# Optimization experiments

Hardware: AMD Instinct MI355X
Metric: run time of the kernel (lower is better)

Reference implementation:

```python
import jax, jax.numpy as jnp
import numpy as np

DIM = 512
HEADS = 8
DIM_HEAD = 64
INNER = HEADS * DIM_HEAD
SCALE = DIM_HEAD ** -0.5


def setup_inputs() -> dict:
    key = jax.random.key(0)
    ks = jax.random.split(key, 7)
    B, N = 8, 1024
    x = jax.random.normal(ks[0], (B, N, DIM), dtype=jnp.float32)
    rel_pos_bias = jax.random.normal(ks[1], (HEADS, N, N), dtype=jnp.float32) * 0.02
    w_qkv = jax.random.normal(ks[2], (DIM, 3 * INNER), dtype=jnp.float32) * (DIM ** -0.5)
    w_out = jax.random.normal(ks[3], (INNER, DIM), dtype=jnp.float32) * (INNER ** -0.5)
    b_out = jnp.zeros((DIM,), dtype=jnp.float32)
    ln_gamma = jnp.ones((DIM,), dtype=jnp.float32)
    ln_beta = jnp.zeros((DIM,), dtype=jnp.float32)
    return {"x": x, "rel_pos_bias": rel_pos_bias, "w_qkv": w_qkv,
            "w_out": w_out, "b_out": b_out, "ln_gamma": ln_gamma, "ln_beta": ln_beta}


def _layernorm(x, gamma, beta, eps=1e-5):
    mu = jnp.mean(x, axis=-1, keepdims=True)
    var = jnp.var(x, axis=-1, keepdims=True)
    return (x - mu) * jax.lax.rsqrt(var + eps) * gamma + beta


def reference(x, rel_pos_bias, w_qkv, w_out, b_out, ln_gamma, ln_beta):
    B, N, _ = x.shape
    xn = _layernorm(x, ln_gamma, ln_beta)
    qkv = xn @ w_qkv  # [B,N,3*INNER]
    q, k, v = jnp.split(qkv, 3, axis=-1)
    # b n (h d) -> b h n d
    reshape = lambda t: t.reshape(B, N, HEADS, DIM_HEAD).transpose(0, 2, 1, 3)
    q, k, v = reshape(q) * SCALE, reshape(k), reshape(v)
    sim = jnp.einsum('bhid,bhjd->bhij', q, k)
    sim = sim + rel_pos_bias  # broadcast [h,N,N] over batch
    attn = jax.nn.softmax(sim, axis=-1)
    out = jnp.einsum('bhij,bhjd->bhid', attn, v)
    out = out.transpose(0, 2, 1, 3).reshape(B, N, INNER)
    return out @ w_out + b_out
```

## Files before the change

### kernel.cpp

```cpp
#include <hip/hip_runtime.h>
#include <hip/hip_bf16.h>

#define DIM 512
#define HEADS 8
#define DHEAD 64
#define INNER 512
#define NSEQ 1024
#define BATCH 8
#define MROWS (BATCH*NSEQ)
#define QK_SCALE 0.125f
#define LOG2E 1.44269504f

typedef __attribute__((ext_vector_type(4))) float f32x4;
typedef __attribute__((ext_vector_type(8))) short short8;
typedef unsigned short ushort_t;

__device__ inline ushort_t f2bf(float f) {
    __hip_bfloat16 h = __float2bfloat16(f);
    return *reinterpret_cast<ushort_t*>(&h);
}
__device__ inline float bf2f(ushort_t u) {
    union { unsigned int i; float f; } c; c.i = ((unsigned int)u) << 16; return c.f;
}
__device__ inline float fast_exp2(float x) {
    float r; asm("v_exp_f32 %0, %1" : "=v"(r) : "v"(x)); return r;
}

#define GLD16(gsrc, ldst) __builtin_amdgcn_global_load_lds( \
    (const __attribute__((address_space(1))) void*)(gsrc), \
    (__attribute__((address_space(3))) void*)(ldst), 16, 0, 0)

__device__ inline void tc_tile(const float* __restrict__ w, ushort_t* __restrict__ wt,
        int ncols, int n0, int k0, int t, ushort_t (*T)[72]) {
    int kr = t >> 2;
    int nc = (t & 3) * 16;
    const float4* src = (const float4*)(w + (size_t)(k0 + kr) * ncols + n0 + nc);
    float4 f0 = src[0], f1 = src[1], f2 = src[2], f3 = src[3];
    ushort_t tmp[16];
    tmp[0]=f2bf(f0.x); tmp[1]=f2bf(f0.y); tmp[2]=f2bf(f0.z); tmp[3]=f2bf(f0.w);
    tmp[4]=f2bf(f1.x); tmp[5]=f2bf(f1.y); tmp[6]=f2bf(f1.z); tmp[7]=f2bf(f1.w);
    tmp[8]=f2bf(f2.x); tmp[9]=f2bf(f2.y); tmp[10]=f2bf(f2.z); tmp[11]=f2bf(f2.w);
    tmp[12]=f2bf(f3.x); tmp[13]=f2bf(f3.y); tmp[14]=f2bf(f3.z); tmp[15]=f2bf(f3.w);
    *(uint4*)&T[kr][nc]     = *(uint4*)&tmp[0];
    *(uint4*)&T[kr][nc + 8] = *(uint4*)&tmp[8];
    __syncthreads();
    int nr = t >> 2;
    int kc = (t & 3) * 16;
    ushort_t o[16];
    for (int j = 0; j < 16; j++) o[j] = T[kc + j][nr];
    ushort_t* dst = wt + (size_t)(n0 + nr) * 512 + k0 + kc;
    *(uint4*)(dst)     = *(uint4*)&o[0];
    *(uint4*)(dst + 8) = *(uint4*)&o[8];
}

__global__ __launch_bounds__(256) void prep_kernel(
        const float* __restrict__ x, const float* __restrict__ gamma,
        const float* __restrict__ beta, ushort_t* __restrict__ xn,
        const float* __restrict__ w_qkv, ushort_t* __restrict__ wqkvT,
        const float* __restrict__ w_out, ushort_t* __restrict__ woutT,
        const float* __restrict__ bias, ushort_t* __restrict__ biasb) {
    __shared__ ushort_t T[64][72];
    int bid = blockIdx.x;
    int t = threadIdx.x;
    if (bid < 2048) {
        int row = bid * 4 + (t >> 6);
        int lane = t & 63;
        const float4* xr = (const float4*)(x + (size_t)row * DIM);
        float4 a0 = xr[lane];
        float4 a1 = xr[lane + 64];
        float s  = a0.x + a0.y + a0.z + a0.w + a1.x + a1.y + a1.z + a1.w;
        float ss = a0.x*a0.x + a0.y*a0.y + a0.z*a0.z + a0.w*a0.w
                 + a1.x*a1.x + a1.y*a1.y + a1.z*a1.z + a1.w*a1.w;
        for (int off = 1; off < 64; off <<= 1) {
            s  += __shfl_xor(s, off);
            ss += __shfl_xor(ss, off);
        }
        float mean = s * (1.0f / DIM);
        float var  = ss * (1.0f / DIM) - mean * mean;
        float inv  = rsqrtf(var + 1e-5f);
        const float4* g4 = (const float4*)gamma;
        const float4* b4 = (const float4*)beta;
        float4 g0 = g4[lane], g1 = g4[lane + 64];
        float4 be0 = b4[lane], be1 = b4[lane + 64];
        ushort4 o0, o1;
        o0.x = f2bf((a0.x - mean) * inv * g0.x + be0.x);
        o0.y = f2bf((a0.y - mean) * inv * g0.y + be0.y);
        o0.z = f2bf((a0.z - mean) * inv * g0.z + be0.z);
        o0.w = f2bf((a0.w - mean) * inv * g0.w + be0.w);
        o1.x = f2bf((a1.x - mean) * inv * g1.x + be1.x);
        o1.y = f2bf((a1.y - mean) * inv * g1.y + be1.y);
        o1.z = f2bf((a1.z - mean) * inv * g1.z + be1.z);
        o1.w = f2bf((a1.w - mean) * inv * g1.w + be1.w);
        ushort4* outr = (ushort4*)(xn + (size_t)row * DIM);
        outr[lane] = o0;
        outr[lane + 64] = o1;
    } else if (bid < 2240) {
        int rel = bid - 2048;
        tc_tile(w_qkv, wqkvT, 1536, (rel % 24) * 64, (rel / 24) * 64, t, T);
    } else if (bid < 2304) {
        int rel = bid - 2240;
        tc_tile(w_out, woutT, 512, (rel % 8) * 64, (rel / 8) * 64, t, T);
    } else {
        int rel = bid - 2304;
        int i = rel * 256 + t;
        float4 v = ((const float4*)bias)[i];
        ushort4 o;
        o.x = f2bf(v.x * LOG2E); o.y = f2bf(v.y * LOG2E);
        o.z = f2bf(v.z * LOG2E); o.w = f2bf(v.w * LOG2E);
        ((ushort4*)biasb)[i] = o;
    }
}

__global__ __launch_bounds__(256) void gemm_qkv(
        const ushort_t* __restrict__ A, const ushort_t* __restrict__ Bt,
        ushort_t* __restrict__ qb, ushort_t* __restrict__ kb, ushort_t* __restrict__ vt) {
    __shared__ ushort_t Als[128][32];
    __shared__ ushort_t Bls[128][32];
    __shared__ ushort_t Tw[4][64][72];
    int t = threadIdx.x, lane = t & 63, w = t >> 6;
    int bm = blockIdx.y, bn = blockIdx.x;
    int wm = w >> 1, wn = w & 1;
    int l15 = lane & 15, l4 = lane >> 4;
    int lr = lane >> 2, lc = (lane & 3) * 8;

    const ushort_t* gA = A  + (size_t)(bm * 128) * DIM;
    const ushort_t* gB = Bt + (size_t)(bn * 128) * DIM;

    f32x4 acc[4][4] = {};

    GLD16(gA + (size_t)(w*32      + lr) * DIM + lc, &Als[w*32][0]);
    GLD16(gA + (size_t)(w*32 + 16 + lr) * DIM + lc, &Als[w*32 + 16][0]);
    GLD16(gB + (size_t)(w*32      + lr) * DIM + lc, &Bls[w*32][0]);
    GLD16(gB + (size_t)(w*32 + 16 + lr) * DIM + lc, &Bls[w*32 + 16][0]);

    for (int kt = 0; kt < DIM / 32; ++kt) {
        __syncthreads();
        short8 af[4], bfr[4];
        for (int mi = 0; mi < 4; mi++) af[mi]  = *(const short8*)&Als[wm*64 + mi*16 + l15][l4*8];
        for (int ni = 0; ni < 4; ni++) bfr[ni] = *(const short8*)&Bls[wn*64 + ni*16 + l15][l4*8];
        __syncthreads();
        if (kt + 1 < DIM / 32) {
            int ko = (kt + 1) * 32;
            GLD16(gA + (size_t)(w*32      + lr) * DIM + ko + lc, &Als[w*32][0]);
            GLD16(gA + (size_t)(w*32 + 16 + lr) * DIM + ko + lc, &Als[w*32 + 16][0]);
            GLD16(gB + (size_t)(w*32      + lr) * DIM + ko + lc, &Bls[w*32][0]);
            GLD16(gB + (size_t)(w*32 + 16 + lr) * DIM + ko + lc, &Bls[w*32 + 16][0]);
        }
        for (int mi = 0; mi < 4; mi++)
            for (int ni = 0; ni < 4; ni++)
                acc[mi][ni] = __builtin_amdgcn_mfma_f32_16x16x32_bf16(bfr[ni], af[mi], acc[mi][ni], 0, 0, 0);
    }

    int c0 = bn*128 + wn*64;
    int part = c0 >> 9;
    int h = (c0 & 511) >> 6;
    int R0 = bm*128 + wm*64;
    int b = R0 >> 10;
    int i0 = R0 & 1023;
    size_t bh = (size_t)(b * HEADS + h);

    if (part == 2) {
        for (int mi = 0; mi < 4; mi++)
            for (int ni = 0; ni < 4; ni++) {
                f32x4 v = acc[mi][ni];
                for (int j = 0; j < 4; j++)
                    Tw[w][ni*16 + l4*4 + j][mi*16 + l15] = f2bf(v[j]);
            }
    } else {
        float qs = (part == 0) ? (QK_SCALE * LOG2E) : 1.0f;
        for (int mi = 0; mi < 4; mi++)
            for (int ni = 0; ni < 4; ni++) {
                f32x4 v = acc[mi][ni];
                ushort4 o;
                o.x = f2bf(v[0] * qs); o.y = f2bf(v[1] * qs);
                o.z = f2bf(v[2] * qs); o.w = f2bf(v[3] * qs);
                *(ushort4*)&Tw[w][mi*16 + l15][ni*16 + l4*4] = o;
            }
    }
    __syncthreads();

    int rr = lane >> 3;
    int cc = (lane & 7) * 8;
    if (part == 2) {
        for (int s = 0; s < 8; s++) {
            int dloc = s*8 + rr;
            uint4 val = *(const uint4*)&Tw[w][dloc][cc];
            *(uint4*)(vt + (bh * DHEAD + dloc) * NSEQ + i0 + cc) = val;
        }
    } else {
        ushort_t* dst = (part == 0) ? qb : kb;
        for (int s = 0; s < 8; s++) {
            int iloc = s*8 + rr;
            uint4 val = *(const uint4*)&Tw[w][iloc][cc];
            *(uint4*)(dst + (bh * NSEQ + (i0 + iloc)) * DHEAD + cc) = val;
        }
    }
}

__global__ __launch_bounds__(256) void gemm_out(
        const ushort_t* __restrict__ A, const ushort_t* __restrict__ Bt,
        float* __restrict__ outp, const float* __restrict__ bvec) {
    __shared__ ushort_t Als[128][32];
    __shared__ ushort_t Bls[64][32];
    __shared__ float Twf[4][64][36];
    int t = threadIdx.x, lane = t & 63, w = t >> 6;
    int bm = blockIdx.y, bn = blockIdx.x;
    int wm = w >> 1, wn = w & 1;
    int l15 = lane & 15, l4 = lane >> 4;
    int lr = lane >> 2, lc = (lane & 3) * 8;

    const ushort_t* gA = A  + (size_t)(bm * 128) * DIM;
    const ushort_t* gB = Bt + (size_t)(bn * 64) * DIM;

    f32x4 acc[4][2] = {};

    GLD16(gA + (size_t)(w*32      + lr) * DIM + lc, &Als[w*32][0]);
    GLD16(gA + (size_t)(w*32 + 16 + lr) * DIM + lc, &Als[w*32 + 16][0]);
    GLD16(gB + (size_t)(w*16 + lr) * DIM + lc, &Bls[w*16][0]);

    for (int kt = 0; kt < DIM / 32; ++kt) {
        __syncthreads();
        short8 af[4], bfr[2];
        for (int mi = 0; mi < 4; mi++) af[mi]  = *(const short8*)&Als[wm*64 + mi*16 + l15][l4*8];
        for (int ni = 0; ni < 2; ni++) bfr[ni] = *(const short8*)&Bls[wn*32 + ni*16 + l15][l4*8];
        __syncthreads();
        if (kt + 1 < DIM / 32) {
            int ko = (kt + 1) * 32;
            GLD16(gA + (size_t)(w*32      + lr) * DIM + ko + lc, &Als[w*32][0]);
            GLD16(gA + (size_t)(w*32 + 16 + lr) * DIM + ko + lc, &Als[w*32 + 16][0]);
            GLD16(gB + (size_t)(w*16 + lr) * DIM + ko + lc, &Bls[w*16][0]);
        }
        for (int mi = 0; mi < 4; mi++)
            for (int ni = 0; ni < 2; ni++)
                acc[mi][ni] = __builtin_amdgcn_mfma_f32_16x16x32_bf16(bfr[ni], af[mi], acc[mi][ni], 0, 0, 0);
    }

    int C0 = bn*64 + wn*32;
    int R0 = bm*128 + wm*64;
    for (int mi = 0; mi < 4; mi++)
        for (int ni = 0; ni < 2; ni++) {
            int c = C0 + ni*16 + l4*4;
            float4 bv = *(const float4*)(bvec + c);
            f32x4 v = acc[mi][ni];
            float4 o2;
            o2.x = v[0] + bv.x; o2.y = v[1] + bv.y;
            o2.z = v[2] + bv.z; o2.w = v[3] + bv.w;
            *(float4*)&Twf[w][mi*16 + l15][ni*16 + l4*4] = o2;
        }
    __syncthreads();

    int rr = lane >> 3;
    int cc = (lane & 7) * 4;
    for (int s = 0; s < 8; s++) {
        int iloc = s*8 + rr;
        float4 val = *(const float4*)&Twf[w][iloc][cc];
        *(float4*)(outp + (size_t)(R0 + iloc) * DIM + C0 + cc) = val;
    }
}

__global__ __launch_bounds__(256) void attn_kernel(
        const ushort_t* __restrict__ q, const ushort_t* __restrict__ k,
        const ushort_t* __restrict__ vt, const ushort_t* __restrict__ biasb,
        ushort_t* __restrict__ attno) {
    __shared__ ushort_t Kls[64][72];
    __shared__ ushort_t Vtls[64][72];
    __shared__ ushort_t Pls[4][16][72];
    int t = threadIdx.x, lane = t & 63, w = t >> 6;
    int l15 = lane & 15, l4 = lane >> 4;
    int bid = blockIdx.x;
    int xcd = bid & 7, s2 = bid >> 3;
    int g = xcd * 16 + (s2 >> 3);
    int b = s2 & 7;
    int h = g & 7;
    int q0 = (g >> 3) * 64;
    size_t bh = (size_t)(b * HEADS + h);
    const ushort_t* qp = q  + (bh * NSEQ + q0 + w*16) * DHEAD;
    const ushort_t* kp = k  + bh * NSEQ * DHEAD;
    const ushort_t* vp = vt + bh * DHEAD * NSEQ;
    int qrow = q0 + w*16 + l15;
    const ushort_t* bp = biasb + ((size_t)h * NSEQ + qrow) * NSEQ;

    short8 bq[2];
    bq[0] = *(const short8*)(qp + l15*DHEAD + l4*8);
    bq[1] = *(const short8*)(qp + l15*DHEAD + l4*8 + 32);

    f32x4 o[4] = {};
    float mrun = -INFINITY, lrun = 0.f;

    int srow = t >> 2, sc = (t & 3) * 16;

    uint4 kreg0, kreg1, vreg0, vreg1;
    ushort4 cb[4], nb[4];
    {
        const ushort_t* ks0 = kp + (size_t)srow * DHEAD + sc;
        const ushort_t* vs0 = vp + (size_t)srow * NSEQ + sc;
        kreg0 = *(const uint4*)(ks0);
        kreg1 = *(const uint4*)(ks0 + 8);
        vreg0 = *(const uint4*)(vs0);
        vreg1 = *(const uint4*)(vs0 + 8);
        for (int ni = 0; ni < 4; ni++)
            cb[ni] = *(const ushort4*)(bp + ni*16 + l4*4);
    }

    for (int kt = 0; kt < NSEQ / 64; ++kt) {
        __syncthreads();
        *(uint4*)&Kls[srow][sc]      = kreg0;
        *(uint4*)&Kls[srow][sc + 8]  = kreg1;
        *(uint4*)&Vtls[srow][sc]     = vreg0;
        *(uint4*)&Vtls[srow][sc + 8] = vreg1;
        __syncthreads();

        if (kt + 1 < NSEQ / 64) {
            const ushort_t* ksn = kp + (size_t)((kt+1)*64 + srow) * DHEAD + sc;
            const ushort_t* vsn = vp + (size_t)srow * NSEQ + (kt+1)*64 + sc;
            kreg0 = *(const uint4*)(ksn);
            kreg1 = *(const uint4*)(ksn + 8);
            vreg0 = *(const uint4*)(vsn);
            vreg1 = *(const uint4*)(vsn + 8);
        }

        f32x4 s[4];
        __builtin_amdgcn_s_setprio(1);
        for (int ni = 0; ni < 4; ni++) {
            f32x4 z = {};
            short8 ak0 = *(const short8*)&Kls[ni*16 + l15][l4*8];
            short8 ak1 = *(const short8*)&Kls[ni*16 + l15][l4*8 + 32];
            z = __builtin_amdgcn_mfma_f32_16x16x32_bf16(ak0, bq[0], z, 0, 0, 0);
            z = __builtin_amdgcn_mfma_f32_16x16x32_bf16(ak1, bq[1], z, 0, 0, 0);
            s[ni] = z;
        }
        __builtin_amdgcn_s_setprio(0);

        float p[16];
        float mj = -INFINITY;
        for (int ni = 0; ni < 4; ni++) {
            ushort4 b4 = cb[ni];
            float v0 = s[ni][0] + bf2f(b4.x);
            float v1 = s[ni][1] + bf2f(b4.y);
            float v2 = s[ni][2] + bf2f(b4.z);
            float v3 = s[ni][3] + bf2f(b4.w);
            p[ni*4+0] = v0; p[ni*4+1] = v1; p[ni*4+2] = v2; p[ni*4+3] = v3;
            mj = fmaxf(mj, fmaxf(fmaxf(v0, v1), fmaxf(v2, v3)));
        }
        mj = fmaxf(mj, __shfl_xor(mj, 16));
        mj = fmaxf(mj, __shfl_xor(mj, 32));
        if (kt + 1 < NSEQ / 64) {
            for (int ni = 0; ni < 4; ni++)
                nb[ni] = *(const ushort4*)(bp + (kt+1)*64 + ni*16 + l4*4);
        }
        if (!__all(mj <= mrun + 8.f)) {
            float mnew = fmaxf(mrun, mj);
            float scl = fast_exp2(mrun - mnew);
            lrun *= scl;
            for (int di = 0; di < 4; di++) o[di] *= scl;
            mrun = mnew;
        }
        float rs = 0.f;
        for (int i = 0; i < 16; i++) {
            p[i] = fast_exp2(p[i] - mrun);
            rs += p[i];
        }
        rs += __shfl_xor(rs, 16);
        rs += __shfl_xor(rs, 32);
        lrun += rs;

        for (int ni = 0; ni < 4; ni++) {
            ushort4 pk;
            pk.x = f2bf(p[ni*4+0]); pk.y = f2bf(p[ni*4+1]);
            pk.z = f2bf(p[ni*4+2]); pk.w = f2bf(p[ni*4+3]);
            *(ushort4*)&Pls[w][l15][ni*16 + l4*4] = pk;
        }

        __builtin_amdgcn_s_setprio(1);
        for (int ks2 = 0; ks2 < 2; ks2++) {
            short8 pb = *(const short8*)&Pls[w][l15][ks2*32 + l4*8];
            for (int di = 0; di < 4; di++) {
                short8 av = *(const short8*)&Vtls[di*16 + l15][ks2*32 + l4*8];
                o[di] = __builtin_amdgcn_mfma_f32_16x16x32_bf16(av, pb, o[di], 0, 0, 0);
            }
        }
        __builtin_amdgcn_s_setprio(0);

        for (int ni = 0; ni < 4; ni++) cb[ni] = nb[ni];
    }

    float inv = 1.0f / lrun;
    for (int di = 0; di < 4; di++) {
        ushort4 ov;
        ov.x = f2bf(o[di][0] * inv);
        ov.y = f2bf(o[di][1] * inv);
        ov.z = f2bf(o[di][2] * inv);
        ov.w = f2bf(o[di][3] * inv);
        *(ushort4*)(attno + ((size_t)(b*NSEQ + qrow)) * INNER + h*DHEAD + di*16 + l4*4) = ov;
    }
}

extern "C" void kernel_launch(void* const* d_in, const int* in_sizes, int n_in,
                              void* d_out, int out_size, void* d_ws, size_t ws_size,
                              hipStream_t stream) {
    (void)in_sizes; (void)n_in; (void)out_size; (void)ws_size;
    const float* x      = (const float*)d_in[0];
    const float* bias   = (const float*)d_in[1];
    const float* w_qkv  = (const float*)d_in[2];
    const float* w_out  = (const float*)d_in[3];
    const float* b_out  = (const float*)d_in[4];
    const float* gamma  = (const float*)d_in[5];
    const float* beta   = (const float*)d_in[6];
    float* out = (float*)d_out;

    ushort_t* xn    = (ushort_t*)d_ws;
    ushort_t* wqkvT = xn + (size_t)MROWS * DIM;
    ushort_t* woutT = wqkvT + (size_t)1536 * 512;
    ushort_t* qb    = woutT + (size_t)512 * 512;
    ushort_t* kb    = qb + (size_t)MROWS * INNER;
    ushort_t* vt    = kb + (size_t)MROWS * INNER;
    ushort_t* attn  = vt + (size_t)MROWS * INNER;
    ushort_t* biasb = attn + (size_t)MROWS * INNER;

    hipLaunchKernelGGL(prep_kernel, dim3(10496), dim3(256), 0, stream,
                       x, gamma, beta, xn, w_qkv, wqkvT, w_out, woutT, bias, biasb);
    hipLaunchKernelGGL(gemm_qkv, dim3(1536 / 128, MROWS / 128), dim3(256), 0, stream,
                       xn, wqkvT, qb, kb, vt);
    hipLaunchKernelGGL(attn_kernel, dim3(BATCH * HEADS * (NSEQ / 64)), dim3(256), 0, stream,
                       qb, kb, vt, biasb, attn);
    hipLaunchKernelGGL(gemm_out, dim3(DIM / 64, MROWS / 128), dim3(256), 0, stream,
                       attn, woutT, out, b_out);
}
```

Baseline: 191.0 us.

## Widen GEMM K-tiles to 64 and enlarge attention KV block with swizzled LDS

Both GEMMs now stage 64-wide K slices per iteration instead of 32, halving the number of loop iterations and barriers. The attention kernel processes 128 keys per step instead of 64. It replaces the padded shared arrays with XOR-swizzled layouts to avoid bank conflicts and folds the bias into the MFMA accumulator init. It also loads bias per tile without prefetch, interleaves P writes with PV MFMAs, and drops the XCD-aware block remapping in favor of a 3D grid. The trade-off is more registers and LDS per block, which may reduce occupancy, and possible loss of L2 locality from the new block ordering.

```diff
diff --git a/kernel.cpp b/kernel.cpp
--- a/kernel.cpp
+++ b/kernel.cpp
@@ -10,6 +10,7 @@
 #define MROWS (BATCH*NSEQ)
 #define QK_SCALE 0.125f
 #define LOG2E 1.44269504f
+#define KVB 128
 
 typedef __attribute__((ext_vector_type(4))) float f32x4;
 typedef __attribute__((ext_vector_type(8))) short short8;
@@ -114,41 +115,44 @@
 __global__ __launch_bounds__(256) void gemm_qkv(
         const ushort_t* __restrict__ A, const ushort_t* __restrict__ Bt,
         ushort_t* __restrict__ qb, ushort_t* __restrict__ kb, ushort_t* __restrict__ vt) {
-    __shared__ ushort_t Als[128][32];
-    __shared__ ushort_t Bls[128][32];
+    __shared__ ushort_t Als[128][64];
+    __shared__ ushort_t Bls[128][64];
     __shared__ ushort_t Tw[4][64][72];
     int t = threadIdx.x, lane = t & 63, w = t >> 6;
     int bm = blockIdx.y, bn = blockIdx.x;
     int wm = w >> 1, wn = w & 1;
     int l15 = lane & 15, l4 = lane >> 4;
-    int lr = lane >> 2, lc = (lane & 3) * 8;
+    int lr8 = lane >> 3, lc8 = (lane & 7) * 8;
 
     const ushort_t* gA = A  + (size_t)(bm * 128) * DIM;
     const ushort_t* gB = Bt + (size_t)(bn * 128) * DIM;
 
     f32x4 acc[4][4] = {};
 
-    GLD16(gA + (size_t)(w*32      + lr) * DIM + lc, &Als[w*32][0]);
-    GLD16(gA + (size_t)(w*32 + 16 + lr) * DIM + lc, &Als[w*32 + 16][0]);
-    GLD16(gB + (size_t)(w*32      + lr) * DIM + lc, &Bls[w*32][0]);
-    GLD16(gB + (size_t)(w*32 + 16 + lr) * DIM + lc, &Bls[w*32 + 16][0]);
-
-    for (int kt = 0; kt < DIM / 32; ++kt) {
-        __syncthreads();
-        short8 af[4], bfr[4];
-        for (int mi = 0; mi < 4; mi++) af[mi]  = *(const short8*)&Als[wm*64 + mi*16 + l15][l4*8];
-        for (int ni = 0; ni < 4; ni++) bfr[ni] = *(const short8*)&Bls[wn*64 + ni*16 + l15][l4*8];
-        __syncthreads();
-        if (kt + 1 < DIM / 32) {
-            int ko = (kt + 1) * 32;
-            GLD16(gA + (size_t)(w*32      + lr) * DIM + ko + lc, &Als[w*32][0]);
-            GLD16(gA + (size_t)(w*32 + 16 + lr) * DIM + ko + lc, &Als[w*32 + 16][0]);
-            GLD16(gB + (size_t)(w*32      + lr) * DIM + ko + lc, &Bls[w*32][0]);
-            GLD16(gB + (size_t)(w*32 + 16 + lr) * DIM + ko + lc, &Bls[w*32 + 16][0]);
-        }
-        for (int mi = 0; mi < 4; mi++)
-            for (int ni = 0; ni < 4; ni++)
-                acc[mi][ni] = __builtin_amdgcn_mfma_f32_16x16x32_bf16(bfr[ni], af[mi], acc[mi][ni], 0, 0, 0);
+    for (int s = 0; s < 4; s++) {
+        GLD16(gA + (size_t)(s*32 + w*8 + lr8) * DIM + lc8, &Als[s*32 + w*8][0]);
+        GLD16(gB + (size_t)(s*32 + w*8 + lr8) * DIM + lc8, &Bls[s*32 + w*8][0]);
+    }
+
+    for (int kt = 0; kt < DIM / 64; ++kt) {
+        __syncthreads();
+        short8 af[2][4], bfr[2][4];
+        for (int ks = 0; ks < 2; ks++) {
+            for (int mi = 0; mi < 4; mi++) af[ks][mi]  = *(const short8*)&Als[wm*64 + mi*16 + l15][ks*32 + l4*8];
+            for (int ni = 0; ni < 4; ni++) bfr[ks][ni] = *(const short8*)&Bls[wn*64 + ni*16 + l15][ks*32 + l4*8];
+        }
+        __syncthreads();
+        if (kt + 1 < DIM / 64) {
+            int ko = (kt + 1) * 64;
+            for (int s = 0; s < 4; s++) {
+                GLD16(gA + (size_t)(s*32 + w*8 + lr8) * DIM + ko + lc8, &Als[s*32 + w*8][0]);
+                GLD16(gB + (size_t)(s*32 + w*8 + lr8) * DIM + ko + lc8, &Bls[s*32 + w*8][0]);
+            }
+        }
+        for (int ks = 0; ks < 2; ks++)
+            for (int mi = 0; mi < 4; mi++)
+                for (int ni = 0; ni < 4; ni++)
+                    acc[mi][ni] = __builtin_amdgcn_mfma_f32_16x16x32_bf16(bfr[ks][ni], af[ks][mi], acc[mi][ni], 0, 0, 0);
     }
 
     int c0 = bn*128 + wn*64;
@@ -200,39 +204,44 @@
 __global__ __launch_bounds__(256) void gemm_out(
         const ushort_t* __restrict__ A, const ushort_t* __restrict__ Bt,
         float* __restrict__ outp, const float* __restrict__ bvec) {
-    __shared__ ushort_t Als[128][32];
-    __shared__ ushort_t Bls[64][32];
+    __shared__ ushort_t Als[128][64];
+    __shared__ ushort_t Bls[64][64];
     __shared__ float Twf[4][64][36];
     int t = threadIdx.x, lane = t & 63, w = t >> 6;
     int bm = blockIdx.y, bn = blockIdx.x;
     int wm = w >> 1, wn = w & 1;
     int l15 = lane & 15, l4 = lane >> 4;
-    int lr = lane >> 2, lc = (lane & 3) * 8;
+    int lr8 = lane >> 3, lc8 = (lane & 7) * 8;
 
     const ushort_t* gA = A  + (size_t)(bm * 128) * DIM;
     const ushort_t* gB = Bt + (size_t)(bn * 64) * DIM;
 
     f32x4 acc[4][2] = {};
 
-    GLD16(gA + (size_t)(w*32      + lr) * DIM + lc, &Als[w*32][0]);
-    GLD16(gA + (size_t)(w*32 + 16 + lr) * DIM + lc, &Als[w*32 + 16][0]);
-    GLD16(gB + (size_t)(w*16 + lr) * DIM + lc, &Bls[w*16][0]);
-
-    for (int kt = 0; kt < DIM / 32; ++kt) {
-        __syncthreads();
-        short8 af[4], bfr[2];
-        for (int mi = 0; mi < 4; mi++) af[mi]  = *(const short8*)&Als[wm*64 + mi*16 + l15][l4*8];
-        for (int ni = 0; ni < 2; ni++) bfr[ni] = *(const short8*)&Bls[wn*32 + ni*16 + l15][l4*8];
-        __syncthreads();
-        if (kt + 1 < DIM / 32) {
-            int ko = (kt + 1) * 32;
-            GLD16(gA + (size_t)(w*32      + lr) * DIM + ko + lc, &Als[w*32][0]);
-            GLD16(gA + (size_t)(w*32 + 16 + lr) * DIM + ko + lc, &Als[w*32 + 16][0]);
-            GLD16(gB + (size_t)(w*16 + lr) * DIM + ko + lc, &Bls[w*16][0]);
-        }
-        for (int mi = 0; mi < 4; mi++)
-            for (int ni = 0; ni < 2; ni++)
-                acc[mi][ni] = __builtin_amdgcn_mfma_f32_16x16x32_bf16(bfr[ni], af[mi], acc[mi][ni], 0, 0, 0);
+    for (int s = 0; s < 4; s++)
+        GLD16(gA + (size_t)(s*32 + w*8 + lr8) * DIM + lc8, &Als[s*32 + w*8][0]);
+    for (int s = 0; s < 2; s++)
+        GLD16(gB + (size_t)(s*32 + w*8 + lr8) * DIM + lc8, &Bls[s*32 + w*8][0]);
+
+    for (int kt = 0; kt < DIM / 64; ++kt) {
+        __syncthreads();
+        short8 af[2][4], bfr[2][2];
+        for (int ks = 0; ks < 2; ks++) {
+            for (int mi = 0; mi < 4; mi++) af[ks][mi]  = *(const short8*)&Als[wm*64 + mi*16 + l15][ks*32 + l4*8];
+            for (int ni = 0; ni < 2; ni++) bfr[ks][ni] = *(const short8*)&Bls[wn*32 + ni*16 + l15][ks*32 + l4*8];
+        }
+        __syncthreads();
+        if (kt + 1 < DIM / 64) {
+            int ko = (kt + 1) * 64;
+            for (int s = 0; s < 4; s++)
+                GLD16(gA + (size_t)(s*32 + w*8 + lr8) * DIM + ko + lc8, &Als[s*32 + w*8][0]);
+            for (int s = 0; s < 2; s++)
+                GLD16(gB + (size_t)(s*32 + w*8 + lr8) * DIM + ko + lc8, &Bls[s*32 + w*8][0]);
+        }
+        for (int ks = 0; ks < 2; ks++)
+            for (int mi = 0; mi < 4; mi++)
+                for (int ni = 0; ni < 2; ni++)
+                    acc[mi][ni] = __builtin_amdgcn_mfma_f32_16x16x32_bf16(bfr[ks][ni], af[ks][mi], acc[mi][ni], 0, 0, 0);
     }
 
     int C0 = bn*64 + wn*32;
@@ -262,17 +271,15 @@
         const ushort_t* __restrict__ q, const ushort_t* __restrict__ k,
         const ushort_t* __restrict__ vt, const ushort_t* __restrict__ biasb,
         ushort_t* __restrict__ attno) {
-    __shared__ ushort_t Kls[64][72];
-    __shared__ ushort_t Vtls[64][72];
-    __shared__ ushort_t Pls[4][16][72];
+    __shared__ ushort_t Kls[128][64];
+    __shared__ ushort_t Vtls[64][128];
+    __shared__ ushort_t Pls[4][16][64];
+    char* Kb = (char*)&Kls[0][0];
+    char* Vb = (char*)&Vtls[0][0];
     int t = threadIdx.x, lane = t & 63, w = t >> 6;
     int l15 = lane & 15, l4 = lane >> 4;
-    int bid = blockIdx.x;
-    int xcd = bid & 7, s2 = bid >> 3;
-    int g = xcd * 16 + (s2 >> 3);
-    int b = s2 & 7;
-    int h = g & 7;
-    int q0 = (g >> 3) * 64;
+    char* Pb = (char*)&Pls[w][0][0];
+    int b = blockIdx.x, h = blockIdx.y, q0 = blockIdx.z * 64;
     size_t bh = (size_t)(b * HEADS + h);
     const ushort_t* qp = q  + (bh * NSEQ + q0 + w*16) * DHEAD;
     const ushort_t* kp = k  + bh * NSEQ * DHEAD;
@@ -287,67 +294,61 @@
     f32x4 o[4] = {};
     float mrun = -INFINITY, lrun = 0.f;
 
-    int srow = t >> 2, sc = (t & 3) * 16;
-
-    uint4 kreg0, kreg1, vreg0, vreg1;
-    ushort4 cb[4], nb[4];
+    int krow = t >> 1;
+    int kce  = (t & 1) * 32;
+    int vrow = t >> 2;
+    int vce  = (t & 3) * 32;
+
+    uint4 kr[4], vr[4];
     {
-        const ushort_t* ks0 = kp + (size_t)srow * DHEAD + sc;
-        const ushort_t* vs0 = vp + (size_t)srow * NSEQ + sc;
-        kreg0 = *(const uint4*)(ks0);
-        kreg1 = *(const uint4*)(ks0 + 8);
-        vreg0 = *(const uint4*)(vs0);
-        vreg1 = *(const uint4*)(vs0 + 8);
-        for (int ni = 0; ni < 4; ni++)
-            cb[ni] = *(const ushort4*)(bp + ni*16 + l4*4);
-    }
-
-    for (int kt = 0; kt < NSEQ / 64; ++kt) {
-        __syncthreads();
-        *(uint4*)&Kls[srow][sc]      = kreg0;
-        *(uint4*)&Kls[srow][sc + 8]  = kreg1;
-        *(uint4*)&Vtls[srow][sc]     = vreg0;
-        *(uint4*)&Vtls[srow][sc + 8] = vreg1;
-        __syncthreads();
-
-        if (kt + 1 < NSEQ / 64) {
-            const ushort_t* ksn = kp + (size_t)((kt+1)*64 + srow) * DHEAD + sc;
-            const ushort_t* vsn = vp + (size_t)srow * NSEQ + (kt+1)*64 + sc;
-            kreg0 = *(const uint4*)(ksn);
-            kreg1 = *(const uint4*)(ksn + 8);
-            vreg0 = *(const uint4*)(vsn);
-            vreg1 = *(const uint4*)(vsn + 8);
-        }
-
-        f32x4 s[4];
+        const ushort_t* ks0 = kp + (size_t)krow * DHEAD + kce;
+        const ushort_t* vs0 = vp + (size_t)vrow * NSEQ + vce;
+        for (int j = 0; j < 4; j++) kr[j] = *(const uint4*)(ks0 + 8*j);
+        for (int j = 0; j < 4; j++) vr[j] = *(const uint4*)(vs0 + 8*j);
+    }
+    int kswz = (krow & 7) << 4;
+    int vswz = (vrow & 15) << 4;
+    int pswz = (l15 & 7) << 4;
+
+    for (int kt = 0; kt < NSEQ / KVB; ++kt) {
+        __syncthreads();
+        for (int j = 0; j < 4; j++)
+            *(uint4*)(Kb + krow*128 + ((kce*2 + 16*j) ^ kswz)) = kr[j];
+        for (int j = 0; j < 4; j++)
+            *(uint4*)(Vb + vrow*256 + ((vce*2 + 16*j) ^ vswz)) = vr[j];
+        __syncthreads();
+
+        if (kt + 1 < NSEQ / KVB) {
+            const ushort_t* ksn = kp + (size_t)((kt+1)*KVB + krow) * DHEAD + kce;
+            const ushort_t* vsn = vp + (size_t)vrow * NSEQ + (kt+1)*KVB + vce;
+            for (int j = 0; j < 4; j++) kr[j] = *(const uint4*)(ksn + 8*j);
+            for (int j = 0; j < 4; j++) vr[j] = *(const uint4*)(vsn + 8*j);
+        }
+
+        ushort4 cb[8];
+        for (int ni = 0; ni < 8; ni++)
+            cb[ni] = *(const ushort4*)(bp + kt*KVB + ni*16 + l4*4);
+
+        f32x4 s[8];
         __builtin_amdgcn_s_setprio(1);
-        for (int ni = 0; ni < 4; ni++) {
-            f32x4 z = {};
-            short8 ak0 = *(const short8*)&Kls[ni*16 + l15][l4*8];
-            short8 ak1 = *(const short8*)&Kls[ni*16 + l15][l4*8 + 32];
-            z = __builtin_amdgcn_mfma_f32_16x16x32_bf16(ak0, bq[0], z, 0, 0, 0);
-            z = __builtin_amdgcn_mfma_f32_16x16x32_bf16(ak1, bq[1], z, 0, 0, 0);
-            s[ni] = z;
+        for (int ni = 0; ni < 8; ni++) {
+            int row = ni*16 + l15;
+            int rsw = (row & 7) << 4;
+            const short8* ka0 = (const short8*)(Kb + row*128 + ((l4*16)      ^ rsw));
+            const short8* ka1 = (const short8*)(Kb + row*128 + ((l4*16 + 64) ^ rsw));
+            f32x4 c0;
+            c0[0] = bf2f(cb[ni].x); c0[1] = bf2f(cb[ni].y);
+            c0[2] = bf2f(cb[ni].z); c0[3] = bf2f(cb[ni].w);
+            f32x4 z = __builtin_amdgcn_mfma_f32_16x16x32_bf16(*ka0, bq[0], c0, 0, 0, 0);
+            s[ni] = __builtin_amdgcn_mfma_f32_16x16x32_bf16(*ka1, bq[1], z, 0, 0, 0);
         }
         __builtin_amdgcn_s_setprio(0);
 
-        float p[16];
         float mj = -INFINITY;
-        for (int ni = 0; ni < 4; ni++) {
-            ushort4 b4 = cb[ni];
-            float v0 = s[ni][0] + bf2f(b4.x);
-            float v1 = s[ni][1] + bf2f(b4.y);
-            float v2 = s[ni][2] + bf2f(b4.z);
-            float v3 = s[ni][3] + bf2f(b4.w);
-            p[ni*4+0] = v0; p[ni*4+1] = v1; p[ni*4+2] = v2; p[ni*4+3] = v3;
-            mj = fmaxf(mj, fmaxf(fmaxf(v0, v1), fmaxf(v2, v3)));
-        }
+        for (int ni = 0; ni < 8; ni++)
+            mj = fmaxf(mj, fmaxf(fmaxf(s[ni][0], s[ni][1]), fmaxf(s[ni][2], s[ni][3])));
         mj = fmaxf(mj, __shfl_xor(mj, 16));
         mj = fmaxf(mj, __shfl_xor(mj, 32));
-        if (kt + 1 < NSEQ / 64) {
-            for (int ni = 0; ni < 4; ni++)
-                nb[ni] = *(const ushort4*)(bp + (kt+1)*64 + ni*16 + l4*4);
-        }
         if (!__all(mj <= mrun + 8.f)) {
             float mnew = fmaxf(mrun, mj);
             float scl = fast_exp2(mrun - mnew);
@@ -356,32 +357,36 @@
             mrun = mnew;
         }
         float rs = 0.f;
-        for (int i = 0; i < 16; i++) {
-            p[i] = fast_exp2(p[i] - mrun);
-            rs += p[i];
-        }
+        for (int ni = 0; ni < 8; ni++)
+            for (int j = 0; j < 4; j++) {
+                float e = fast_exp2(s[ni][j] - mrun);
+                s[ni][j] = e;
+                rs += e;
+            }
         rs += __shfl_xor(rs, 16);
         rs += __shfl_xor(rs, 32);
         lrun += rs;
 
-        for (int ni = 0; ni < 4; ni++) {
-            ushort4 pk;
-            pk.x = f2bf(p[ni*4+0]); pk.y = f2bf(p[ni*4+1]);
-            pk.z = f2bf(p[ni*4+2]); pk.w = f2bf(p[ni*4+3]);
-            *(ushort4*)&Pls[w][l15][ni*16 + l4*4] = pk;
-        }
-
         __builtin_amdgcn_s_setprio(1);
-        for (int ks2 = 0; ks2 < 2; ks2++) {
-            short8 pb = *(const short8*)&Pls[w][l15][ks2*32 + l4*8];
-            for (int di = 0; di < 4; di++) {
-                short8 av = *(const short8*)&Vtls[di*16 + l15][ks2*32 + l4*8];
-                o[di] = __builtin_amdgcn_mfma_f32_16x16x32_bf16(av, pb, o[di], 0, 0, 0);
+        for (int h2 = 0; h2 < 2; h2++) {
+            for (int nii = 0; nii < 4; nii++) {
+                int ni = h2*4 + nii;
+                ushort4 pk;
+                pk.x = f2bf(s[ni][0]); pk.y = f2bf(s[ni][1]);
+                pk.z = f2bf(s[ni][2]); pk.w = f2bf(s[ni][3]);
+                *(ushort4*)(Pb + l15*128 + ((nii*32 + l4*8) ^ pswz)) = pk;
+            }
+            for (int ks = 0; ks < 2; ks++) {
+                const short8* pb8 = (const short8*)(Pb + l15*128 + ((ks*64 + l4*16) ^ pswz));
+                short8 pbv = *pb8;
+                for (int di = 0; di < 4; di++) {
+                    int vrw = di*16 + l15;
+                    const short8* av = (const short8*)(Vb + vrw*256 + (((h2*2+ks)*64 + l4*16) ^ ((vrw & 15) << 4)));
+                    o[di] = __builtin_amdgcn_mfma_f32_16x16x32_bf16(*av, pbv, o[di], 0, 0, 0);
+                }
             }
         }
         __builtin_amdgcn_s_setprio(0);
-
-        for (int ni = 0; ni < 4; ni++) cb[ni] = nb[ni];
     }
 
     float inv = 1.0f / lrun;
@@ -421,7 +426,7 @@
                        x, gamma, beta, xn, w_qkv, wqkvT, w_out, woutT, bias, biasb);
     hipLaunchKernelGGL(gemm_qkv, dim3(1536 / 128, MROWS / 128), dim3(256), 0, stream,
                        xn, wqkvT, qb, kb, vt);
-    hipLaunchKernelGGL(attn_kernel, dim3(BATCH * HEADS * (NSEQ / 64)), dim3(256), 0, stream,
+    hipLaunchKernelGGL(attn_kernel, dim3(BATCH, HEADS, NSEQ / 64), dim3(256), 0, stream,
                        qb, kb, vt, biasb, attn);
     hipLaunchKernelGGL(gemm_out, dim3(DIM / 64, MROWS / 128), dim3(256), 0, stream,
                        attn, woutT, out, b_out);
```

After: 254.1 us. 33.0% more time.
